# Optimization experiments

Measured on AMD Instinct MI355X. Metric: run time of the kernel, lower is better.

Reference implementation:

```python
import jax, jax.numpy as jnp
import numpy as np

MIN_EXP = 1    # log2(min_window=2)
MAX_EXP = 10   # log2(max_window=1024)
OUT_LEN = 16384  # reconstructed signal length L; encoded len = L*(1 - 2**-MAX_EXP)


def setup_inputs() -> dict:
    key = jax.random.key(0)
    k1, k2, k3 = jax.random.split(key, 3)
    B = 2048
    enc_len = OUT_LEN * (2 ** (1 - MIN_EXP)) - OUT_LEN // (2 ** MAX_EXP)  # 16368
    weights_len = 2 * (2 ** MAX_EXP) - 1  # 2047
    stdev = 1.0 / np.sqrt(weights_len)
    data = jax.random.normal(k1, (B, enc_len), dtype=jnp.float32)
    weights = jax.random.uniform(k2, (weights_len,), dtype=jnp.float32, minval=-stdev, maxval=stdev)
    bias = jax.random.uniform(k3, (MAX_EXP,), dtype=jnp.float32, minval=-stdev, maxval=stdev)
    return {"data": data, "weights": weights, "bias": bias}


def reference(data, weights, bias):
    """Transposed time-scale convolution: for each dyadic scale e (window w=2**e),
    the shared kernel weights[w-1:2w-1] is overlap-added (stride == window, so the
    windows tile the output exactly) scaled by that scale's coefficients, summed
    across scales, with a per-scale bias."""
    B = data.shape[0]
    out = jnp.zeros((B, OUT_LEN), dtype=data.dtype)
    offset = 0
    for e in range(MIN_EXP, MAX_EXP + 1):
        w = 2 ** e
        n = OUT_LEN // w                      # number of windows at this scale
        kern = weights[w - 1: 2 * w - 1]      # [w] kernel for this scale
        coeffs = data[:, offset: offset + n]  # [B, n]
        offset += n
        # transposed conv with stride = kernel size: outer product then tile
        contrib = (coeffs[:, :, None] * kern[None, None, :]).reshape(B, OUT_LEN)
        out = out + contrib + bias[e - 1]
    return out
```

## Files before the change

### kernel.cpp

```cpp
#include <hip/hip_runtime.h>
#include <hip/hip_bf16.h>

#define TSC_OUT_LEN 16384
#define TSC_ENC_LEN 16368

__global__ __launch_bounds__(256) void tsc_transpose_kernel(
    const float* __restrict__ data,
    const float* __restrict__ weights,
    const float* __restrict__ bias,
    float* __restrict__ out)
{
    __shared__ float wl[2048];
    const int tid = threadIdx.x;
    for (int i = tid; i < 2047; i += 256) wl[i + 1] = weights[i];
    if (tid == 0) wl[0] = 0.0f;
    __syncthreads();

    float bs = 0.0f;
#pragma unroll
    for (int i = 0; i < 10; ++i) bs += bias[i];

    const int b    = blockIdx.x >> 3;
    const int tile = (blockIdx.x & 7) << 11;
    const int j0   = tile + (tid << 3);
    const float* drow = data + (size_t)b * TSC_ENC_LEN;

    float acc[8];
#pragma unroll
    for (int k = 0; k < 8; ++k) acc[k] = bs;

    {
        const float4 d4 = *reinterpret_cast<const float4*>(drow + (j0 >> 1));
        const float w1 = wl[2], w2 = wl[3];
        acc[0] += d4.x * w1; acc[1] += d4.x * w2;
        acc[2] += d4.y * w1; acc[3] += d4.y * w2;
        acc[4] += d4.z * w1; acc[5] += d4.z * w2;
        acc[6] += d4.w * w1; acc[7] += d4.w * w2;
    }
    {
        const float2 d2 = *reinterpret_cast<const float2*>(drow + 8192 + (j0 >> 2));
        const float4 kv = *reinterpret_cast<const float4*>(&wl[4]);
        acc[0] += d2.x * kv.x; acc[1] += d2.x * kv.y;
        acc[2] += d2.x * kv.z; acc[3] += d2.x * kv.w;
        acc[4] += d2.y * kv.x; acc[5] += d2.y * kv.y;
        acc[6] += d2.y * kv.z; acc[7] += d2.y * kv.w;
    }
#pragma unroll
    for (int e = 3; e <= 10; ++e) {
        const int w   = 1 << e;
        const int off = TSC_OUT_LEN - (TSC_OUT_LEN >> (e - 1));
        const float c = drow[off + (j0 >> e)];
        const int  kb = w + (j0 & (w - 1));
        const float4 k0 = *reinterpret_cast<const float4*>(&wl[kb]);
        const float4 k1 = *reinterpret_cast<const float4*>(&wl[kb + 4]);
        acc[0] += c * k0.x; acc[1] += c * k0.y;
        acc[2] += c * k0.z; acc[3] += c * k0.w;
        acc[4] += c * k1.x; acc[5] += c * k1.y;
        acc[6] += c * k1.z; acc[7] += c * k1.w;
    }

    float4* o = reinterpret_cast<float4*>(out + (size_t)b * TSC_OUT_LEN + j0);
    o[0] = make_float4(acc[0], acc[1], acc[2], acc[3]);
    o[1] = make_float4(acc[4], acc[5], acc[6], acc[7]);
}

extern "C" void kernel_launch(void* const* d_in, const int* in_sizes, int n_in,
                              void* d_out, int out_size, void* d_ws, size_t ws_size,
                              hipStream_t stream) {
    const float* data    = (const float*)d_in[0];
    const float* weights = (const float*)d_in[1];
    const float* bias    = (const float*)d_in[2];
    float* out = (float*)d_out;

    const int B = in_sizes[0] / TSC_ENC_LEN;
    dim3 grid(B * 8);
    dim3 block(256);
    tsc_transpose_kernel<<<grid, block, 0, stream>>>(data, weights, bias, out);
}
```

Before: 235.7 us.

## Retile to 16 outputs per thread with swizzled weight LDS and staged coarse coefficients

Each block now covers half an output row with 512 threads, and each thread produces 16 contiguous outputs instead of 8. This cuts the grid from 8 to 2 blocks per batch row, so the per-block weight staging into LDS is amortised over more outputs. The weights are stored in LDS with a padded swizzle to reduce bank conflicts on the float4 reads. The coarse-scale coefficients are staged cooperatively into LDS so threads share them instead of issuing scattered scalar global loads. The trade-off is fewer blocks and higher register use per thread, which can lower occupancy.

```diff
diff --git a/kernel.cpp b/kernel.cpp
--- a/kernel.cpp
+++ b/kernel.cpp
@@ -4,64 +4,123 @@
 #define TSC_OUT_LEN 16384
 #define TSC_ENC_LEN 16368
 
-__global__ __launch_bounds__(256) void tsc_transpose_kernel(
+
+__device__ __forceinline__ int swz(int g) { return g + 4 * (g >> 4); }
+
+__global__ __launch_bounds__(512) void tsc_transpose_kernel(
     const float* __restrict__ data,
     const float* __restrict__ weights,
     const float* __restrict__ bias,
     float* __restrict__ out)
 {
-    __shared__ float wl[2048];
+    __shared__ __align__(16) float wl[2560];
+    __shared__ __align__(16) float dl[1024];
+
     const int tid = threadIdx.x;
-    for (int i = tid; i < 2047; i += 256) wl[i + 1] = weights[i];
-    if (tid == 0) wl[0] = 0.0f;
+    const int t   = blockIdx.x & 1;
+    const int b   = blockIdx.x >> 1;
+    const float* drow = data + (size_t)b * TSC_ENC_LEN;
+
+    if (tid < 511) {
+        const float4 w4 = *reinterpret_cast<const float4*>(weights + 4 * tid);
+        const int g = 4 * tid + 1;
+        wl[swz(g)]     = w4.x;
+        wl[swz(g + 1)] = w4.y;
+        wl[swz(g + 2)] = w4.z;
+        wl[swz(g + 3)] = w4.w;
+    } else {
+        wl[swz(2045)] = weights[2044];
+        wl[swz(2046)] = weights[2045];
+        wl[swz(2047)] = weights[2046];
+    }
+
+    if (tid < 254) {
+        const int c = (tid >= 128) + (tid >= 192) + (tid >= 224) +
+                      (tid >= 240) + (tid >= 248) + (tid >= 252);
+        const int q   = tid - (256 - (256 >> c));
+        const int src = 16384 - (2048 >> c) + t * (512 >> c) + 4 * q;
+        const int dst = 1024 - (1024 >> c) + 4 * q;
+        const float4 v = *reinterpret_cast<const float4*>(drow + src);
+        *reinterpret_cast<float4*>(&dl[dst]) = v;
+    }
     __syncthreads();
 
-    float bs = 0.0f;
-#pragma unroll
-    for (int i = 0; i < 10; ++i) bs += bias[i];
+    float bs = bias[0] + bias[1] + bias[2] + bias[3] + bias[4] +
+               bias[5] + bias[6] + bias[7] + bias[8] + bias[9];
 
-    const int b    = blockIdx.x >> 3;
-    const int tile = (blockIdx.x & 7) << 11;
-    const int j0   = tile + (tid << 3);
-    const float* drow = data + (size_t)b * TSC_ENC_LEN;
+    const int j0 = t * 8192 + tid * 16;
 
-    float acc[8];
-#pragma unroll
-    for (int k = 0; k < 8; ++k) acc[k] = bs;
+    const float4 d1a = *reinterpret_cast<const float4*>(drow + t * 4096 + 8 * tid);
+    const float4 d1b = *reinterpret_cast<const float4*>(drow + t * 4096 + 8 * tid + 4);
+    const float4 d2  = *reinterpret_cast<const float4*>(drow + 8192 + t * 2048 + 4 * tid);
+    const float2 d3  = *reinterpret_cast<const float2*>(drow + 12288 + t * 1024 + 2 * tid);
+
+    float cds[7];
+    cds[0] = dl[tid];
+    cds[1] = dl[512  + (tid >> 1)];
+    cds[2] = dl[768  + (tid >> 2)];
+    cds[3] = dl[896  + (tid >> 3)];
+    cds[4] = dl[960  + (tid >> 4)];
+    cds[5] = dl[992  + (tid >> 5)];
+    cds[6] = dl[1008 + (tid >> 6)];
+
+    float acc[16];
 
     {
-        const float4 d4 = *reinterpret_cast<const float4*>(drow + (j0 >> 1));
         const float w1 = wl[2], w2 = wl[3];
-        acc[0] += d4.x * w1; acc[1] += d4.x * w2;
-        acc[2] += d4.y * w1; acc[3] += d4.y * w2;
-        acc[4] += d4.z * w1; acc[5] += d4.z * w2;
-        acc[6] += d4.w * w1; acc[7] += d4.w * w2;
+        const float d1[8] = {d1a.x, d1a.y, d1a.z, d1a.w, d1b.x, d1b.y, d1b.z, d1b.w};
+#pragma unroll
+        for (int k = 0; k < 16; ++k)
+            acc[k] = bs + d1[k >> 1] * ((k & 1) ? w2 : w1);
     }
     {
-        const float2 d2 = *reinterpret_cast<const float2*>(drow + 8192 + (j0 >> 2));
-        const float4 kv = *reinterpret_cast<const float4*>(&wl[4]);
-        acc[0] += d2.x * kv.x; acc[1] += d2.x * kv.y;
-        acc[2] += d2.x * kv.z; acc[3] += d2.x * kv.w;
-        acc[4] += d2.y * kv.x; acc[5] += d2.y * kv.y;
-        acc[6] += d2.y * kv.z; acc[7] += d2.y * kv.w;
+        const float4 kf = *reinterpret_cast<const float4*>(&wl[4]);
+        const float kw[4] = {kf.x, kf.y, kf.z, kf.w};
+        const float dd[4] = {d2.x, d2.y, d2.z, d2.w};
+#pragma unroll
+        for (int k = 0; k < 16; ++k)
+            acc[k] += dd[k >> 2] * kw[k & 3];
+    }
+    {
+        const float4 ka = *reinterpret_cast<const float4*>(&wl[8]);
+        const float4 kb = *reinterpret_cast<const float4*>(&wl[12]);
+        const float kw[8] = {ka.x, ka.y, ka.z, ka.w, kb.x, kb.y, kb.z, kb.w};
+        const float dd[2] = {d3.x, d3.y};
+#pragma unroll
+        for (int k = 0; k < 16; ++k)
+            acc[k] += dd[k >> 3] * kw[k & 7];
+    }
+    {
+        const float4 f0 = *reinterpret_cast<const float4*>(&wl[20]);
+        const float4 f1 = *reinterpret_cast<const float4*>(&wl[24]);
+        const float4 f2 = *reinterpret_cast<const float4*>(&wl[28]);
+        const float4 f3 = *reinterpret_cast<const float4*>(&wl[32]);
+        const float c4 = cds[0];
+        acc[0]  += c4 * f0.x; acc[1]  += c4 * f0.y; acc[2]  += c4 * f0.z; acc[3]  += c4 * f0.w;
+        acc[4]  += c4 * f1.x; acc[5]  += c4 * f1.y; acc[6]  += c4 * f1.z; acc[7]  += c4 * f1.w;
+        acc[8]  += c4 * f2.x; acc[9]  += c4 * f2.y; acc[10] += c4 * f2.z; acc[11] += c4 * f2.w;
+        acc[12] += c4 * f3.x; acc[13] += c4 * f3.y; acc[14] += c4 * f3.z; acc[15] += c4 * f3.w;
     }
 #pragma unroll
-    for (int e = 3; e <= 10; ++e) {
-        const int w   = 1 << e;
-        const int off = TSC_OUT_LEN - (TSC_OUT_LEN >> (e - 1));
-        const float c = drow[off + (j0 >> e)];
-        const int  kb = w + (j0 & (w - 1));
-        const float4 k0 = *reinterpret_cast<const float4*>(&wl[kb]);
-        const float4 k1 = *reinterpret_cast<const float4*>(&wl[kb + 4]);
-        acc[0] += c * k0.x; acc[1] += c * k0.y;
-        acc[2] += c * k0.z; acc[3] += c * k0.w;
-        acc[4] += c * k1.x; acc[5] += c * k1.y;
-        acc[6] += c * k1.z; acc[7] += c * k1.w;
+    for (int e = 5; e <= 10; ++e) {
+        const int g0 = (1 << e) + ((tid & ((1 << (e - 4)) - 1)) << 4);
+        const int a0 = swz(g0);
+        const float4 f0 = *reinterpret_cast<const float4*>(&wl[a0]);
+        const float4 f1 = *reinterpret_cast<const float4*>(&wl[a0 + 4]);
+        const float4 f2 = *reinterpret_cast<const float4*>(&wl[a0 + 8]);
+        const float4 f3 = *reinterpret_cast<const float4*>(&wl[a0 + 12]);
+        const float ce = cds[e - 4];
+        acc[0]  += ce * f0.x; acc[1]  += ce * f0.y; acc[2]  += ce * f0.z; acc[3]  += ce * f0.w;
+        acc[4]  += ce * f1.x; acc[5]  += ce * f1.y; acc[6]  += ce * f1.z; acc[7]  += ce * f1.w;
+        acc[8]  += ce * f2.x; acc[9]  += ce * f2.y; acc[10] += ce * f2.z; acc[11] += ce * f2.w;
+        acc[12] += ce * f3.x; acc[13] += ce * f3.y; acc[14] += ce * f3.z; acc[15] += ce * f3.w;
     }
 
     float4* o = reinterpret_cast<float4*>(out + (size_t)b * TSC_OUT_LEN + j0);
-    o[0] = make_float4(acc[0], acc[1], acc[2], acc[3]);
-    o[1] = make_float4(acc[4], acc[5], acc[6], acc[7]);
+    o[0] = make_float4(acc[0],  acc[1],  acc[2],  acc[3]);
+    o[1] = make_float4(acc[4],  acc[5],  acc[6],  acc[7]);
+    o[2] = make_float4(acc[8],  acc[9],  acc[10], acc[11]);
+    o[3] = make_float4(acc[12], acc[13], acc[14], acc[15]);
 }
 
 extern "C" void kernel_launch(void* const* d_in, const int* in_sizes, int n_in,
@@ -73,7 +132,7 @@
     float* out = (float*)d_out;
 
     const int B = in_sizes[0] / TSC_ENC_LEN;
-    dim3 grid(B * 8);
-    dim3 block(256);
+    dim3 grid(B * 2);
+    dim3 block(512);
     tsc_transpose_kernel<<<grid, block, 0, stream>>>(data, weights, bias, out);
 }
```

Result: slower. 241.5 us (+2.4%).
